# Kernel optimization log

Hardware: AMD Instinct MI355X
Metric: run time of the kernel (lower is better)

## Reference

```python
import jax, jax.numpy as jnp
import numpy as np

BATCH = 131072
FEAS = 256
K = 256
DEPTH = 3


def setup_inputs() -> dict:
    key = jax.random.key(0)
    ks = jax.random.split(key, 16)
    # deep tower dims: k//1 -> k//2 -> k//3 -> k//4  == 256 -> 128 -> 85 -> 64
    dims = [K // i for i in range(1, DEPTH + 2)]
    inp = {
        "x": jax.random.normal(ks[0], (BATCH, FEAS), jnp.float32),
        "w_wide": jax.random.normal(ks[1], (FEAS, 1), jnp.float32) * 0.02,
        "b_wide": jnp.zeros((1,), jnp.float32),
        # nn.Parameter(torch.rand(feas, k)) -> uniform [0,1)
        "V": jax.random.uniform(ks[2], (FEAS, K), jnp.float32),
    }
    for i in range(DEPTH):
        fan_in, fan_out = dims[i], dims[i + 1]
        inp[f"w{i+1}"] = jax.random.normal(ks[3 + 2 * i], (fan_in, fan_out), jnp.float32) * (1.0 / np.sqrt(fan_in))
        inp[f"b{i+1}"] = jnp.zeros((fan_out,), jnp.float32)
    inp["w_out"] = jax.random.normal(ks[12], (dims[-1], 1), jnp.float32) * (1.0 / np.sqrt(dims[-1]))
    inp["b_out"] = jnp.zeros((1,), jnp.float32)
    return inp


def reference(x, w_wide, b_wide, V, w1, b1, w2, b2, w3, b3, w_out, b_out):
    # wide (linear) part: [B, 1]
    linear = x @ w_wide + b_wide
    # FM bi-interaction pooling. Original loop: sum_{j >= i} x_i x_j (v_i * v_j)
    # (break/continue on zeros only skip zero-valued terms). Including the
    # diagonal, this equals 0.5 * ((x @ V)^2 + (x^2) @ (V^2)).  [B, K]
    xv = x @ V
    x2v2 = (x * x) @ (V * V)
    tmp = 0.5 * (xv * xv + x2v2)
    # deep tower: Linear + ReLU at each depth
    for w, b in ((w1, b1), (w2, b2), (w3, b3)):
        tmp = jax.nn.relu(tmp @ w + b)
    deep_out = tmp @ w_out + b_out  # [B, 1]
    return jax.nn.sigmoid(linear + deep_out)
```

## Files before the change

kernel.cpp:

```cpp
#include <hip/hip_runtime.h>
#include <math.h>


typedef _Float16 f16;
typedef _Float16 f16x4 __attribute__((ext_vector_type(4)));
typedef _Float16 f16x8 __attribute__((ext_vector_type(8)));
typedef float f32x4 __attribute__((ext_vector_type(4)));

#define NROWS   131072
#define ROWS    64
#define FDIM    256
#define KDIM    256
#define D1      128
#define D2      85
#define D2P     96
#define D3      64

#define OFF_VT_H   0x0UL
#define OFF_VT_L   0x20000UL
#define OFF_V2T    0x40000UL
#define OFF_W1T_H  0x60000UL
#define OFF_W1T_L  0x70000UL
#define OFF_W2T_H  0x80000UL
#define OFF_W2T_L  0x86000UL
#define OFF_W3T_H  0x8C000UL
#define OFF_W3T_L  0x8F000UL
#define OFF_LIN    0x92000UL

static __device__ __forceinline__ f32x4 mfma16(f16x8 a, f16x8 b, f32x4 c) {
  return __builtin_amdgcn_mfma_f32_16x16x32_f16(a, b, c, 0, 0, 0);
}

__global__ __launch_bounds__(256) void prep_kernel(
    const float* __restrict__ V, const float* __restrict__ w1,
    const float* __restrict__ w2, const float* __restrict__ w3,
    f16* VT_h, f16* VT_l, f16* V2T,
    f16* W1T_h, f16* W1T_l, f16* W2T_h, f16* W2T_l, f16* W3T_h, f16* W3T_l) {
  int idx0 = blockIdx.x * 256 + threadIdx.x;
  int stride = gridDim.x * 256;
  for (int idx = idx0; idx < KDIM * FDIM; idx += stride) {
    int k = idx >> 8, i = idx & 255;
    float v = V[i * KDIM + k];
    f16 h = (f16)v;
    VT_h[idx] = h;
    VT_l[idx] = (f16)(v - (float)h);
    V2T[idx] = (f16)(v * v);
  }
  for (int idx = idx0; idx < D1 * KDIM; idx += stride) {
    int n = idx >> 8, k = idx & 255;
    float w = w1[k * D1 + n];
    f16 h = (f16)w;
    W1T_h[idx] = h;
    W1T_l[idx] = (f16)(w - (float)h);
  }
  for (int idx = idx0; idx < D2P * D1; idx += stride) {
    int n = idx >> 7, k = idx & 127;
    float w = (n < D2) ? w2[k * D2 + n] : 0.f;
    f16 h = (f16)w;
    W2T_h[idx] = h;
    W2T_l[idx] = (f16)(w - (float)h);
  }
  for (int idx = idx0; idx < D3 * D2P; idx += stride) {
    int n = idx / D2P, k = idx - n * D2P;
    float w = (k < D2) ? w3[k * D3 + n] : 0.f;
    f16 h = (f16)w;
    W3T_h[idx] = h;
    W3T_l[idx] = (f16)(w - (float)h);
  }
}

__global__ __launch_bounds__(256, 2) void fused_kernel(
    const float* __restrict__ x, const float* __restrict__ w_wide,
    const float* __restrict__ b_wide,
    const f16* __restrict__ VT_h, const f16* __restrict__ VT_l,
    const f16* __restrict__ V2T,
    const f16* __restrict__ W1T_h, const f16* __restrict__ W1T_l,
    const float* __restrict__ b1,
    const f16* __restrict__ W2T_h, const f16* __restrict__ W2T_l,
    const float* __restrict__ b2,
    const f16* __restrict__ W3T_h, const f16* __restrict__ W3T_l,
    const float* __restrict__ b3,
    const float* __restrict__ w_out, const float* __restrict__ b_out,
    float* __restrict__ lin_g, float* __restrict__ out) {
  __shared__ __align__(16) f16 smem[32768];

  f16* tmpH = smem;
  f16* tmpL = smem + 16384;
  f16* sXh  = smem;
  f16* sXl  = smem + 2560;
  f16* sX2  = smem + 5120;
  f16* h1H  = smem + 16384;
  f16* h1L  = smem + 24576;
  f16* h2H  = smem;
  f16* h2L  = smem + 8192;

  const int tid = threadIdx.x;
  const int lane = tid & 63, wv = tid >> 6;
  const int q = lane >> 4, ln = lane & 15;
  const int row0 = blockIdx.x * ROWS;
  const int sr = tid >> 3, sc = (tid & 7) * 4;

  f32x4 accV[4][4], acc2[4][4];
#pragma unroll
  for (int i = 0; i < 4; ++i)
#pragma unroll
    for (int j = 0; j < 4; ++j) {
      accV[i][j] = (f32x4){0.f, 0.f, 0.f, 0.f};
      acc2[i][j] = (f32x4){0.f, 0.f, 0.f, 0.f};
    }
  float lin0 = 0.f, lin1 = 0.f;

  for (int ks = 0; ks < 8; ++ks) {
    const int k0 = ks * 32;
    float4 a0 = *(const float4*)(x + (size_t)(row0 + sr) * FDIM + k0 + sc);
    float4 a1 = *(const float4*)(x + (size_t)(row0 + sr + 32) * FDIM + k0 + sc);
    float4 w4 = *(const float4*)(w_wide + k0 + sc);
    lin0 += a0.x * w4.x + a0.y * w4.y + a0.z * w4.z + a0.w * w4.w;
    lin1 += a1.x * w4.x + a1.y * w4.y + a1.z * w4.z + a1.w * w4.w;

    __syncthreads();
    {
      float f0[4] = {a0.x, a0.y, a0.z, a0.w};
      float f1[4] = {a1.x, a1.y, a1.z, a1.w};
      f16x4 h0, l0, q0, h1v, l1v, q1v;
#pragma unroll
      for (int j = 0; j < 4; ++j) {
        f16 h = (f16)f0[j];
        h0[j] = h; l0[j] = (f16)(f0[j] - (float)h); q0[j] = (f16)(f0[j] * f0[j]);
        f16 g = (f16)f1[j];
        h1v[j] = g; l1v[j] = (f16)(f1[j] - (float)g); q1v[j] = (f16)(f1[j] * f1[j]);
      }
      int off0 = sr * 40 + sc, off1 = (sr + 32) * 40 + sc;
      *(f16x4*)(sXh + off0) = h0; *(f16x4*)(sXl + off0) = l0; *(f16x4*)(sX2 + off0) = q0;
      *(f16x4*)(sXh + off1) = h1v; *(f16x4*)(sXl + off1) = l1v; *(f16x4*)(sX2 + off1) = q1v;
    }
    __syncthreads();

    f16x8 Ah[4], Al[4], A2[4];
#pragma unroll
    for (int mi = 0; mi < 4; ++mi) {
      int off = (mi * 16 + ln) * 40 + q * 8;
      Ah[mi] = *(const f16x8*)(sXh + off);
      Al[mi] = *(const f16x8*)(sXl + off);
      A2[mi] = *(const f16x8*)(sX2 + off);
    }
#pragma unroll
    for (int ni = 0; ni < 4; ++ni) {
      int n = wv * 64 + ni * 16 + ln;
      size_t boff = (size_t)n * FDIM + k0 + q * 8;
      f16x8 Bh = *(const f16x8*)(VT_h + boff);
      f16x8 Bl = *(const f16x8*)(VT_l + boff);
      f16x8 B2 = *(const f16x8*)(V2T + boff);
#pragma unroll
      for (int mi = 0; mi < 4; ++mi) {
        accV[mi][ni] = mfma16(Al[mi], Bh, accV[mi][ni]);
        accV[mi][ni] = mfma16(Ah[mi], Bl, accV[mi][ni]);
        accV[mi][ni] = mfma16(Ah[mi], Bh, accV[mi][ni]);
        acc2[mi][ni] = mfma16(A2[mi], B2, acc2[mi][ni]);
      }
    }
  }

  {
    float bw = b_wide[0];
    float s0 = lin0, s1 = lin1;
    s0 += __shfl_xor(s0, 1); s0 += __shfl_xor(s0, 2); s0 += __shfl_xor(s0, 4);
    s1 += __shfl_xor(s1, 1); s1 += __shfl_xor(s1, 2); s1 += __shfl_xor(s1, 4);
    if ((tid & 7) == 0) {
      lin_g[row0 + sr] = s0 + bw;
      lin_g[row0 + sr + 32] = s1 + bw;
    }
  }

  __syncthreads();

#pragma unroll
  for (int mi = 0; mi < 4; ++mi)
#pragma unroll
    for (int r = 0; r < 4; ++r) {
      int m = mi * 16 + q * 4 + r;
      int mrow = m * 256, msw = m & 7;
#pragma unroll
      for (int ni = 0; ni < 4; ++ni) {
        int n = wv * 64 + ni * 16 + ln;
        float xv = accV[mi][ni][r];
        float val = 0.5f * (xv * xv + acc2[mi][ni][r]);
        f16 hi = (f16)val;
        f16 lo = (f16)(val - (float)hi);
        int off = mrow + (((n >> 3) ^ msw) << 3) + (n & 7);
        tmpH[off] = hi;
        tmpL[off] = lo;
      }
    }

  __syncthreads();

  f32x4 acc1[4][2];
#pragma unroll
  for (int i = 0; i < 4; ++i) { acc1[i][0] = (f32x4){0,0,0,0}; acc1[i][1] = (f32x4){0,0,0,0}; }

#pragma unroll
  for (int ks = 0; ks < 8; ++ks) {
    f16x8 Ah[4], Al[4];
#pragma unroll
    for (int mi = 0; mi < 4; ++mi) {
      int m = mi * 16 + ln;
      int off = m * 256 + (((ks * 4 + q) ^ (m & 7)) << 3);
      Ah[mi] = *(const f16x8*)(tmpH + off);
      Al[mi] = *(const f16x8*)(tmpL + off);
    }
#pragma unroll
    for (int ni = 0; ni < 2; ++ni) {
      int n = wv * 32 + ni * 16 + ln;
      size_t boff = (size_t)n * KDIM + ks * 32 + q * 8;
      f16x8 Bh = *(const f16x8*)(W1T_h + boff);
      f16x8 Bl = *(const f16x8*)(W1T_l + boff);
#pragma unroll
      for (int mi = 0; mi < 4; ++mi) {
        acc1[mi][ni] = mfma16(Al[mi], Bh, acc1[mi][ni]);
        acc1[mi][ni] = mfma16(Ah[mi], Bl, acc1[mi][ni]);
        acc1[mi][ni] = mfma16(Ah[mi], Bh, acc1[mi][ni]);
      }
    }
  }

  __syncthreads();

#pragma unroll
  for (int mi = 0; mi < 4; ++mi)
#pragma unroll
    for (int r = 0; r < 4; ++r) {
      int m = mi * 16 + q * 4 + r;
      int mrow = m * 128, msw = m & 7;
#pragma unroll
      for (int ni = 0; ni < 2; ++ni) {
        int n = wv * 32 + ni * 16 + ln;
        float z = acc1[mi][ni][r] + b1[n];
        z = z > 0.f ? z : 0.f;
        f16 hi = (f16)z;
        f16 lo = (f16)(z - (float)hi);
        int off = mrow + (((n >> 3) ^ msw) << 3) + (n & 7);
        h1H[off] = hi;
        h1L[off] = lo;
      }
    }

  __syncthreads();

  f32x4 accL2[6];
#pragma unroll
  for (int j = 0; j < 6; ++j) accL2[j] = (f32x4){0, 0, 0, 0};

#pragma unroll
  for (int ks = 0; ks < 4; ++ks) {
    int m = wv * 16 + ln;
    int aoff = m * 128 + (((ks * 4 + q) ^ (m & 7)) << 3);
    f16x8 Ah = *(const f16x8*)(h1H + aoff);
    f16x8 Al = *(const f16x8*)(h1L + aoff);
#pragma unroll
    for (int ni = 0; ni < 6; ++ni) {
      int n = ni * 16 + ln;
      size_t boff = (size_t)n * D1 + ks * 32 + q * 8;
      f16x8 Bh = *(const f16x8*)(W2T_h + boff);
      f16x8 Bl = *(const f16x8*)(W2T_l + boff);
      accL2[ni] = mfma16(Al, Bh, accL2[ni]);
      accL2[ni] = mfma16(Ah, Bl, accL2[ni]);
      accL2[ni] = mfma16(Ah, Bh, accL2[ni]);
    }
  }

#pragma unroll
  for (int r = 0; r < 4; ++r) {
    int m = wv * 16 + q * 4 + r;
    int mrow = m * 128, msw = m & 7;
#pragma unroll
    for (int ni = 0; ni < 6; ++ni) {
      int n = ni * 16 + ln;
      float z = accL2[ni][r] + ((n < D2) ? b2[n] : 0.f);
      z = z > 0.f ? z : 0.f;
      f16 hi = (f16)z;
      f16 lo = (f16)(z - (float)hi);
      int off = mrow + (((n >> 3) ^ msw) << 3) + (n & 7);
      h2H[off] = hi;
      h2L[off] = lo;
    }
  }

  __syncthreads();

  f32x4 accL3[4];
#pragma unroll
  for (int j = 0; j < 4; ++j) accL3[j] = (f32x4){0, 0, 0, 0};

#pragma unroll
  for (int ks = 0; ks < 3; ++ks) {
    int m = wv * 16 + ln;
    int aoff = m * 128 + (((ks * 4 + q) ^ (m & 7)) << 3);
    f16x8 Ah = *(const f16x8*)(h2H + aoff);
    f16x8 Al = *(const f16x8*)(h2L + aoff);
#pragma unroll
    for (int ni = 0; ni < 4; ++ni) {
      int n = ni * 16 + ln;
      size_t boff = (size_t)n * D2P + ks * 32 + q * 8;
      f16x8 Bh = *(const f16x8*)(W3T_h + boff);
      f16x8 Bl = *(const f16x8*)(W3T_l + boff);
      accL3[ni] = mfma16(Al, Bh, accL3[ni]);
      accL3[ni] = mfma16(Ah, Bl, accL3[ni]);
      accL3[ni] = mfma16(Ah, Bh, accL3[ni]);
    }
  }

  {
    float b3v[4], wov[4];
#pragma unroll
    for (int ni = 0; ni < 4; ++ni) {
      int n = ni * 16 + ln;
      b3v[ni] = b3[n];
      wov[ni] = w_out[n];
    }
    float bo = b_out[0];
#pragma unroll
    for (int r = 0; r < 4; ++r) {
      float part = 0.f;
#pragma unroll
      for (int ni = 0; ni < 4; ++ni) {
        float z = accL3[ni][r] + b3v[ni];
        part += (z > 0.f ? z : 0.f) * wov[ni];
      }
      part += __shfl_xor(part, 1);
      part += __shfl_xor(part, 2);
      part += __shfl_xor(part, 4);
      part += __shfl_xor(part, 8);
      if (ln == 0) {
        int m = row0 + wv * 16 + q * 4 + r;
        float lv = *((volatile const float*)(lin_g + m));
        float zf = lv + part + bo;
        out[m] = 1.f / (1.f + expf(-zf));
      }
    }
  }
}

extern "C" void kernel_launch(void* const* d_in, const int* in_sizes, int n_in,
                              void* d_out, int out_size, void* d_ws, size_t ws_size,
                              hipStream_t stream) {
  const float* x = (const float*)d_in[0];
  const float* w_wide = (const float*)d_in[1];
  const float* b_wide = (const float*)d_in[2];
  const float* V = (const float*)d_in[3];
  const float* w1 = (const float*)d_in[4];
  const float* b1 = (const float*)d_in[5];
  const float* w2 = (const float*)d_in[6];
  const float* b2 = (const float*)d_in[7];
  const float* w3 = (const float*)d_in[8];
  const float* b3 = (const float*)d_in[9];
  const float* w_out = (const float*)d_in[10];
  const float* b_out = (const float*)d_in[11];
  float* out = (float*)d_out;
  char* ws = (char*)d_ws;

  f16* VT_h = (f16*)(ws + OFF_VT_H);
  f16* VT_l = (f16*)(ws + OFF_VT_L);
  f16* V2T = (f16*)(ws + OFF_V2T);
  f16* W1T_h = (f16*)(ws + OFF_W1T_H);
  f16* W1T_l = (f16*)(ws + OFF_W1T_L);
  f16* W2T_h = (f16*)(ws + OFF_W2T_H);
  f16* W2T_l = (f16*)(ws + OFF_W2T_L);
  f16* W3T_h = (f16*)(ws + OFF_W3T_H);
  f16* W3T_l = (f16*)(ws + OFF_W3T_L);
  float* lin_g = (float*)(ws + OFF_LIN);

  prep_kernel<<<64, 256, 0, stream>>>(V, w1, w2, w3, VT_h, VT_l, V2T, W1T_h,
                                      W1T_l, W2T_h, W2T_l, W3T_h, W3T_l);

  fused_kernel<<<NROWS / ROWS, 256, 0, stream>>>(
      x, w_wide, b_wide, VT_h, VT_l, V2T, W1T_h, W1T_l, b1, W2T_h, W2T_l, b2,
      W3T_h, W3T_l, b3, w_out, b_out, lin_g, out);
}
```

Before: 400.1 us.

## Use 512-thread blocks, prefetch x tiles, keep linear term in LDS

Doubles the workgroup to 512 threads (8 waves) per 64-row tile and splits each GEMM stage's N dimension across more waves, cutting the accumulator registers each wave holds. The next x slice is loaded into registers while the current one is used, to overlap global loads with MFMA work. The wide linear term and the two halves of the final dot product now go through shared memory, so the global scratch write and read-back are gone. With 8 waves there are fewer tiles per wave and more barrier traffic, and the launch-bounds change alters how the compiler allocates registers.

After: 405.0 us. About the same (+1.2%).

```diff
diff --git a/kernel.cpp b/kernel.cpp
--- a/kernel.cpp
+++ b/kernel.cpp
@@ -14,7 +14,6 @@
 #define D1      128
 #define D2      85
 #define D2P     96
-#define D3      64
 
 #define OFF_VT_H   0x0UL
 #define OFF_VT_L   0x20000UL
@@ -25,7 +24,6 @@
 #define OFF_W2T_L  0x86000UL
 #define OFF_W3T_H  0x8C000UL
 #define OFF_W3T_L  0x8F000UL
-#define OFF_LIN    0x92000UL
 
 static __device__ __forceinline__ f32x4 mfma16(f16x8 a, f16x8 b, f32x4 c) {
   return __builtin_amdgcn_mfma_f32_16x16x32_f16(a, b, c, 0, 0, 0);
@@ -60,16 +58,16 @@
     W2T_h[idx] = h;
     W2T_l[idx] = (f16)(w - (float)h);
   }
-  for (int idx = idx0; idx < D3 * D2P; idx += stride) {
+  for (int idx = idx0; idx < 64 * D2P; idx += stride) {
     int n = idx / D2P, k = idx - n * D2P;
-    float w = (k < D2) ? w3[k * D3 + n] : 0.f;
+    float w = (k < D2) ? w3[k * 64 + n] : 0.f;
     f16 h = (f16)w;
     W3T_h[idx] = h;
     W3T_l[idx] = (f16)(w - (float)h);
   }
 }
 
-__global__ __launch_bounds__(256, 2) void fused_kernel(
+__global__ __launch_bounds__(512, 4) void fused_kernel(
     const float* __restrict__ x, const float* __restrict__ w_wide,
     const float* __restrict__ b_wide,
     const f16* __restrict__ VT_h, const f16* __restrict__ VT_l,
@@ -81,8 +79,10 @@
     const f16* __restrict__ W3T_h, const f16* __restrict__ W3T_l,
     const float* __restrict__ b3,
     const float* __restrict__ w_out, const float* __restrict__ b_out,
-    float* __restrict__ lin_g, float* __restrict__ out) {
+    float* __restrict__ out) {
   __shared__ __align__(16) f16 smem[32768];
+  __shared__ float linS[ROWS];
+  __shared__ float pfS[ROWS * 2];
 
   f16* tmpH = smem;
   f16* tmpL = smem + 16384;
@@ -100,76 +100,81 @@
   const int row0 = blockIdx.x * ROWS;
   const int sr = tid >> 3, sc = (tid & 7) * 4;
 
-  f32x4 accV[4][4], acc2[4][4];
+  f32x4 accV[4][2], acc2[4][2];
 #pragma unroll
   for (int i = 0; i < 4; ++i)
 #pragma unroll
-    for (int j = 0; j < 4; ++j) {
+    for (int j = 0; j < 2; ++j) {
       accV[i][j] = (f32x4){0.f, 0.f, 0.f, 0.f};
       acc2[i][j] = (f32x4){0.f, 0.f, 0.f, 0.f};
     }
-  float lin0 = 0.f, lin1 = 0.f;
+  float linp = 0.f;
+
+  const float* xrow = x + (size_t)(row0 + sr) * FDIM + sc;
+  float4 a_cur = *(const float4*)(xrow);
+  float4 w_cur = *(const float4*)(w_wide + sc);
 
   for (int ks = 0; ks < 8; ++ks) {
     const int k0 = ks * 32;
-    float4 a0 = *(const float4*)(x + (size_t)(row0 + sr) * FDIM + k0 + sc);
-    float4 a1 = *(const float4*)(x + (size_t)(row0 + sr + 32) * FDIM + k0 + sc);
-    float4 w4 = *(const float4*)(w_wide + k0 + sc);
-    lin0 += a0.x * w4.x + a0.y * w4.y + a0.z * w4.z + a0.w * w4.w;
-    lin1 += a1.x * w4.x + a1.y * w4.y + a1.z * w4.z + a1.w * w4.w;
-
     __syncthreads();
     {
-      float f0[4] = {a0.x, a0.y, a0.z, a0.w};
-      float f1[4] = {a1.x, a1.y, a1.z, a1.w};
-      f16x4 h0, l0, q0, h1v, l1v, q1v;
+      float f0[4] = {a_cur.x, a_cur.y, a_cur.z, a_cur.w};
+      f16x4 h0, l0, q0;
 #pragma unroll
       for (int j = 0; j < 4; ++j) {
         f16 h = (f16)f0[j];
-        h0[j] = h; l0[j] = (f16)(f0[j] - (float)h); q0[j] = (f16)(f0[j] * f0[j]);
-        f16 g = (f16)f1[j];
-        h1v[j] = g; l1v[j] = (f16)(f1[j] - (float)g); q1v[j] = (f16)(f1[j] * f1[j]);
-      }
-      int off0 = sr * 40 + sc, off1 = (sr + 32) * 40 + sc;
-      *(f16x4*)(sXh + off0) = h0; *(f16x4*)(sXl + off0) = l0; *(f16x4*)(sX2 + off0) = q0;
-      *(f16x4*)(sXh + off1) = h1v; *(f16x4*)(sXl + off1) = l1v; *(f16x4*)(sX2 + off1) = q1v;
+        h0[j] = h;
+        l0[j] = (f16)(f0[j] - (float)h);
+        q0[j] = (f16)(f0[j] * f0[j]);
+      }
+      int off0 = sr * 40 + sc;
+      *(f16x4*)(sXh + off0) = h0;
+      *(f16x4*)(sXl + off0) = l0;
+      *(f16x4*)(sX2 + off0) = q0;
     }
     __syncthreads();
 
-    f16x8 Ah[4], Al[4], A2[4];
+    float4 a_nxt = a_cur, w_nxt = w_cur;
+    if (ks < 7) {
+      a_nxt = *(const float4*)(xrow + k0 + 32);
+      w_nxt = *(const float4*)(w_wide + k0 + 32 + sc);
+    }
+    linp += a_cur.x * w_cur.x + a_cur.y * w_cur.y + a_cur.z * w_cur.z +
+            a_cur.w * w_cur.w;
+
+    f16x8 Bh[2], Bl[2], B2[2];
+#pragma unroll
+    for (int ni = 0; ni < 2; ++ni) {
+      int n = wv * 32 + ni * 16 + ln;
+      size_t boff = (size_t)n * FDIM + k0 + q * 8;
+      Bh[ni] = *(const f16x8*)(VT_h + boff);
+      Bl[ni] = *(const f16x8*)(VT_l + boff);
+      B2[ni] = *(const f16x8*)(V2T + boff);
+    }
 #pragma unroll
     for (int mi = 0; mi < 4; ++mi) {
       int off = (mi * 16 + ln) * 40 + q * 8;
-      Ah[mi] = *(const f16x8*)(sXh + off);
-      Al[mi] = *(const f16x8*)(sXl + off);
-      A2[mi] = *(const f16x8*)(sX2 + off);
-    }
-#pragma unroll
-    for (int ni = 0; ni < 4; ++ni) {
-      int n = wv * 64 + ni * 16 + ln;
-      size_t boff = (size_t)n * FDIM + k0 + q * 8;
-      f16x8 Bh = *(const f16x8*)(VT_h + boff);
-      f16x8 Bl = *(const f16x8*)(VT_l + boff);
-      f16x8 B2 = *(const f16x8*)(V2T + boff);
-#pragma unroll
-      for (int mi = 0; mi < 4; ++mi) {
-        accV[mi][ni] = mfma16(Al[mi], Bh, accV[mi][ni]);
-        accV[mi][ni] = mfma16(Ah[mi], Bl, accV[mi][ni]);
-        accV[mi][ni] = mfma16(Ah[mi], Bh, accV[mi][ni]);
-        acc2[mi][ni] = mfma16(A2[mi], B2, acc2[mi][ni]);
-      }
-    }
+      f16x8 Ah = *(const f16x8*)(sXh + off);
+      f16x8 Al = *(const f16x8*)(sXl + off);
+      f16x8 A2 = *(const f16x8*)(sX2 + off);
+#pragma unroll
+      for (int ni = 0; ni < 2; ++ni) {
+        accV[mi][ni] = mfma16(Al, Bh[ni], accV[mi][ni]);
+        accV[mi][ni] = mfma16(Ah, Bl[ni], accV[mi][ni]);
+        accV[mi][ni] = mfma16(Ah, Bh[ni], accV[mi][ni]);
+        acc2[mi][ni] = mfma16(A2, B2[ni], acc2[mi][ni]);
+      }
+    }
+    a_cur = a_nxt;
+    w_cur = w_nxt;
   }
 
   {
-    float bw = b_wide[0];
-    float s0 = lin0, s1 = lin1;
-    s0 += __shfl_xor(s0, 1); s0 += __shfl_xor(s0, 2); s0 += __shfl_xor(s0, 4);
-    s1 += __shfl_xor(s1, 1); s1 += __shfl_xor(s1, 2); s1 += __shfl_xor(s1, 4);
-    if ((tid & 7) == 0) {
-      lin_g[row0 + sr] = s0 + bw;
-      lin_g[row0 + sr + 32] = s1 + bw;
-    }
+    float s0 = linp;
+    s0 += __shfl_xor(s0, 1);
+    s0 += __shfl_xor(s0, 2);
+    s0 += __shfl_xor(s0, 4);
+    if ((tid & 7) == 0) linS[sr] = s0 + b_wide[0];
   }
 
   __syncthreads();
@@ -181,8 +186,8 @@
       int m = mi * 16 + q * 4 + r;
       int mrow = m * 256, msw = m & 7;
 #pragma unroll
-      for (int ni = 0; ni < 4; ++ni) {
-        int n = wv * 64 + ni * 16 + ln;
+      for (int ni = 0; ni < 2; ++ni) {
+        int n = wv * 32 + ni * 16 + ln;
         float xv = accV[mi][ni][r];
         float val = 0.5f * (xv * xv + acc2[mi][ni][r]);
         f16 hi = (f16)val;
@@ -195,88 +200,80 @@
 
   __syncthreads();
 
-  f32x4 acc1[4][2];
-#pragma unroll
-  for (int i = 0; i < 4; ++i) { acc1[i][0] = (f32x4){0,0,0,0}; acc1[i][1] = (f32x4){0,0,0,0}; }
+  f32x4 acc1[4];
+#pragma unroll
+  for (int i = 0; i < 4; ++i) acc1[i] = (f32x4){0.f, 0.f, 0.f, 0.f};
 
 #pragma unroll
   for (int ks = 0; ks < 8; ++ks) {
-    f16x8 Ah[4], Al[4];
+    size_t boff = (size_t)(wv * 16 + ln) * KDIM + ks * 32 + q * 8;
+    f16x8 Bh = *(const f16x8*)(W1T_h + boff);
+    f16x8 Bl = *(const f16x8*)(W1T_l + boff);
 #pragma unroll
     for (int mi = 0; mi < 4; ++mi) {
       int m = mi * 16 + ln;
-      int off = m * 256 + (((ks * 4 + q) ^ (m & 7)) << 3);
-      Ah[mi] = *(const f16x8*)(tmpH + off);
-      Al[mi] = *(const f16x8*)(tmpL + off);
-    }
-#pragma unroll
-    for (int ni = 0; ni < 2; ++ni) {
-      int n = wv * 32 + ni * 16 + ln;
-      size_t boff = (size_t)n * KDIM + ks * 32 + q * 8;
-      f16x8 Bh = *(const f16x8*)(W1T_h + boff);
-      f16x8 Bl = *(const f16x8*)(W1T_l + boff);
-#pragma unroll
-      for (int mi = 0; mi < 4; ++mi) {
-        acc1[mi][ni] = mfma16(Al[mi], Bh, acc1[mi][ni]);
-        acc1[mi][ni] = mfma16(Ah[mi], Bl, acc1[mi][ni]);
-        acc1[mi][ni] = mfma16(Ah[mi], Bh, acc1[mi][ni]);
-      }
-    }
-  }
-
-  __syncthreads();
-
-#pragma unroll
-  for (int mi = 0; mi < 4; ++mi)
-#pragma unroll
-    for (int r = 0; r < 4; ++r) {
-      int m = mi * 16 + q * 4 + r;
-      int mrow = m * 128, msw = m & 7;
-#pragma unroll
-      for (int ni = 0; ni < 2; ++ni) {
-        int n = wv * 32 + ni * 16 + ln;
-        float z = acc1[mi][ni][r] + b1[n];
+      int aoff = m * 256 + (((ks * 4 + q) ^ (m & 7)) << 3);
+      f16x8 Ah = *(const f16x8*)(tmpH + aoff);
+      f16x8 Al = *(const f16x8*)(tmpL + aoff);
+      acc1[mi] = mfma16(Al, Bh, acc1[mi]);
+      acc1[mi] = mfma16(Ah, Bl, acc1[mi]);
+      acc1[mi] = mfma16(Ah, Bh, acc1[mi]);
+    }
+  }
+
+  __syncthreads();
+
+  {
+    int n = wv * 16 + ln;
+    float bias = b1[n];
+#pragma unroll
+    for (int mi = 0; mi < 4; ++mi)
+#pragma unroll
+      for (int r = 0; r < 4; ++r) {
+        int m = mi * 16 + q * 4 + r;
+        float z = acc1[mi][r] + bias;
         z = z > 0.f ? z : 0.f;
         f16 hi = (f16)z;
         f16 lo = (f16)(z - (float)hi);
-        int off = mrow + (((n >> 3) ^ msw) << 3) + (n & 7);
+        int off = m * 128 + (((n >> 3) ^ (m & 7)) << 3) + (n & 7);
         h1H[off] = hi;
         h1L[off] = lo;
       }
-    }
-
-  __syncthreads();
-
-  f32x4 accL2[6];
-#pragma unroll
-  for (int j = 0; j < 6; ++j) accL2[j] = (f32x4){0, 0, 0, 0};
+  }
+
+  __syncthreads();
+
+  const int mt = wv & 3, half = wv >> 2;
+  f32x4 accL2[3];
+#pragma unroll
+  for (int j = 0; j < 3; ++j) accL2[j] = (f32x4){0.f, 0.f, 0.f, 0.f};
 
 #pragma unroll
   for (int ks = 0; ks < 4; ++ks) {
-    int m = wv * 16 + ln;
+    int m = mt * 16 + ln;
     int aoff = m * 128 + (((ks * 4 + q) ^ (m & 7)) << 3);
     f16x8 Ah = *(const f16x8*)(h1H + aoff);
     f16x8 Al = *(const f16x8*)(h1L + aoff);
 #pragma unroll
-    for (int ni = 0; ni < 6; ++ni) {
-      int n = ni * 16 + ln;
+    for (int nj = 0; nj < 3; ++nj) {
+      int n = (half * 3 + nj) * 16 + ln;
       size_t boff = (size_t)n * D1 + ks * 32 + q * 8;
       f16x8 Bh = *(const f16x8*)(W2T_h + boff);
       f16x8 Bl = *(const f16x8*)(W2T_l + boff);
-      accL2[ni] = mfma16(Al, Bh, accL2[ni]);
-      accL2[ni] = mfma16(Ah, Bl, accL2[ni]);
-      accL2[ni] = mfma16(Ah, Bh, accL2[ni]);
+      accL2[nj] = mfma16(Al, Bh, accL2[nj]);
+      accL2[nj] = mfma16(Ah, Bl, accL2[nj]);
+      accL2[nj] = mfma16(Ah, Bh, accL2[nj]);
     }
   }
 
 #pragma unroll
   for (int r = 0; r < 4; ++r) {
-    int m = wv * 16 + q * 4 + r;
+    int m = mt * 16 + q * 4 + r;
     int mrow = m * 128, msw = m & 7;
 #pragma unroll
-    for (int ni = 0; ni < 6; ++ni) {
-      int n = ni * 16 + ln;
-      float z = accL2[ni][r] + ((n < D2) ? b2[n] : 0.f);
+    for (int nj = 0; nj < 3; ++nj) {
+      int n = (half * 3 + nj) * 16 + ln;
+      float z = accL2[nj][r] + ((n < D2) ? b2[n] : 0.f);
       z = z > 0.f ? z : 0.f;
       f16 hi = (f16)z;
       f16 lo = (f16)(z - (float)hi);
@@ -288,56 +285,57 @@
 
   __syncthreads();
 
-  f32x4 accL3[4];
-#pragma unroll
-  for (int j = 0; j < 4; ++j) accL3[j] = (f32x4){0, 0, 0, 0};
+  f32x4 accL3[2];
+  accL3[0] = (f32x4){0.f, 0.f, 0.f, 0.f};
+  accL3[1] = (f32x4){0.f, 0.f, 0.f, 0.f};
 
 #pragma unroll
   for (int ks = 0; ks < 3; ++ks) {
-    int m = wv * 16 + ln;
+    int m = mt * 16 + ln;
     int aoff = m * 128 + (((ks * 4 + q) ^ (m & 7)) << 3);
     f16x8 Ah = *(const f16x8*)(h2H + aoff);
     f16x8 Al = *(const f16x8*)(h2L + aoff);
 #pragma unroll
-    for (int ni = 0; ni < 4; ++ni) {
-      int n = ni * 16 + ln;
+    for (int nj = 0; nj < 2; ++nj) {
+      int n = (half * 2 + nj) * 16 + ln;
       size_t boff = (size_t)n * D2P + ks * 32 + q * 8;
       f16x8 Bh = *(const f16x8*)(W3T_h + boff);
       f16x8 Bl = *(const f16x8*)(W3T_l + boff);
-      accL3[ni] = mfma16(Al, Bh, accL3[ni]);
-      accL3[ni] = mfma16(Ah, Bl, accL3[ni]);
-      accL3[ni] = mfma16(Ah, Bh, accL3[ni]);
+      accL3[nj] = mfma16(Al, Bh, accL3[nj]);
+      accL3[nj] = mfma16(Ah, Bl, accL3[nj]);
+      accL3[nj] = mfma16(Ah, Bh, accL3[nj]);
     }
   }
 
   {
-    float b3v[4], wov[4];
-#pragma unroll
-    for (int ni = 0; ni < 4; ++ni) {
-      int n = ni * 16 + ln;
-      b3v[ni] = b3[n];
-      wov[ni] = w_out[n];
-    }
-    float bo = b_out[0];
+    float b3v[2], wov[2];
+#pragma unroll
+    for (int nj = 0; nj < 2; ++nj) {
+      int n = (half * 2 + nj) * 16 + ln;
+      b3v[nj] = b3[n];
+      wov[nj] = w_out[n];
+    }
 #pragma unroll
     for (int r = 0; r < 4; ++r) {
       float part = 0.f;
 #pragma unroll
-      for (int ni = 0; ni < 4; ++ni) {
-        float z = accL3[ni][r] + b3v[ni];
-        part += (z > 0.f ? z : 0.f) * wov[ni];
+      for (int nj = 0; nj < 2; ++nj) {
+        float z = accL3[nj][r] + b3v[nj];
+        part += (z > 0.f ? z : 0.f) * wov[nj];
       }
       part += __shfl_xor(part, 1);
       part += __shfl_xor(part, 2);
       part += __shfl_xor(part, 4);
       part += __shfl_xor(part, 8);
-      if (ln == 0) {
-        int m = row0 + wv * 16 + q * 4 + r;
-        float lv = *((volatile const float*)(lin_g + m));
-        float zf = lv + part + bo;
-        out[m] = 1.f / (1.f + expf(-zf));
-      }
-    }
+      if (ln == 0) pfS[(mt * 16 + q * 4 + r) * 2 + half] = part;
+    }
+  }
+
+  __syncthreads();
+
+  if (tid < ROWS) {
+    float zf = linS[tid] + pfS[tid * 2] + pfS[tid * 2 + 1] + b_out[0];
+    out[row0 + tid] = 1.f / (1.f + expf(-zf));
   }
 }
 
@@ -368,12 +366,11 @@
   f16* W2T_l = (f16*)(ws + OFF_W2T_L);
   f16* W3T_h = (f16*)(ws + OFF_W3T_H);
   f16* W3T_l = (f16*)(ws + OFF_W3T_L);
-  float* lin_g = (float*)(ws + OFF_LIN);
 
   prep_kernel<<<64, 256, 0, stream>>>(V, w1, w2, w3, VT_h, VT_l, V2T, W1T_h,
                                       W1T_l, W2T_h, W2T_l, W3T_h, W3T_l);
 
-  fused_kernel<<<NROWS / ROWS, 256, 0, stream>>>(
+  fused_kernel<<<NROWS / ROWS, 512, 0, stream>>>(
       x, w_wide, b_wide, VT_h, VT_l, V2T, W1T_h, W1T_l, b1, W2T_h, W2T_l, b2,
-      W3T_h, W3T_l, b3, w_out, b_out, lin_g, out);
+      W3T_h, W3T_l, b3, w_out, b_out, out);
 }
```
